# Kernel optimization log

Hardware: AMD Instinct MI355X
Metric: run time of the kernel (lower is better)

The kernel has to match this reference:

```python
import jax, jax.numpy as jnp
import numpy as np

IN_F = 8192
OUT_F = 8192
TOKENS = 4096
QP = 127.0   # 2**(8-1) - 1
QN = -128.0  # -2**(8-1)


def setup_inputs() -> dict:
    key = jax.random.key(0)
    k1, k2 = jax.random.split(key)
    x = jax.random.normal(k1, (TOKENS, IN_F), dtype=jnp.float32)
    # torch.randint(0, 2, ...) -> values in {0, 1}
    weight = jax.random.randint(k2, (OUT_F, IN_F), 0, 2, dtype=jnp.int32)
    weight_scale = jnp.ones((1,), dtype=jnp.float32)
    bias = jnp.zeros((OUT_F,), dtype=jnp.float32)
    return {"x": x, "weight": weight, "weight_scale": weight_scale, "bias": bias}


def reference(x, weight, weight_scale, bias):
    # activation_quant: per-row symmetric int8 quantization
    s = QP / jnp.clip(jnp.max(jnp.abs(x), axis=-1, keepdims=True), 1e-5)  # [T,1]
    x_q = jnp.clip(jnp.round(x * s), QN, QP)  # int8 values held in f32 (exact)
    y = jnp.einsum('tk,nk->tn', x_q, weight.astype(x.dtype))  # [T, OUT_F]
    # post_quant_process: dequantize by activation scale then weight scale
    out = y / s / weight_scale
    return out + bias[None, :]
```

## Files before the change

### kernel.cpp

```cpp
#include <hip/hip_runtime.h>

#define TOKENS 4096
#define IN_F   8192
#define OUT_F  8192

typedef int v4i __attribute__((ext_vector_type(4)));

__device__ __forceinline__ void gload_lds16(const void* g, void* l) {
    __builtin_amdgcn_global_load_lds(
        (const __attribute__((address_space(1))) void*)g,
        (__attribute__((address_space(3))) void*)l, 16, 0, 0);
}

__global__ __launch_bounds__(256) void quant_kernel(const float* __restrict__ x,
                                                    signed char* __restrict__ xq,
                                                    float* __restrict__ recip_s) {
    const int row = blockIdx.x;
    const int t   = threadIdx.x;
    const float4* xr = (const float4*)(x + (size_t)row * IN_F);
    float4 v[8];
    float m = 0.f;
#pragma unroll
    for (int i = 0; i < 8; ++i) {
        v[i] = xr[t + 256 * i];
        m = fmaxf(m, fmaxf(fmaxf(fabsf(v[i].x), fabsf(v[i].y)),
                           fmaxf(fabsf(v[i].z), fabsf(v[i].w))));
    }
#pragma unroll
    for (int off = 32; off > 0; off >>= 1)
        m = fmaxf(m, __shfl_xor(m, off));
    __shared__ float wmax[4];
    if ((t & 63) == 0) wmax[t >> 6] = m;
    __syncthreads();
    m = fmaxf(fmaxf(wmax[0], wmax[1]), fmaxf(wmax[2], wmax[3]));
    m = fmaxf(m, 1e-5f);
    const float s = 127.0f / m;
    if (t == 0) recip_s[row] = m / 127.0f;
    unsigned int* out = (unsigned int*)(xq + (size_t)row * IN_F);
#pragma unroll
    for (int i = 0; i < 8; ++i) {
        int a = (int)fminf(fmaxf(rintf(v[i].x * s), -128.f), 127.f);
        int b = (int)fminf(fmaxf(rintf(v[i].y * s), -128.f), 127.f);
        int c = (int)fminf(fmaxf(rintf(v[i].z * s), -128.f), 127.f);
        int d = (int)fminf(fmaxf(rintf(v[i].w * s), -128.f), 127.f);
        out[t + 256 * i] = (a & 255) | ((b & 255) << 8) | ((c & 255) << 16) | ((d & 255) << 24);
    }
}

__global__ __launch_bounds__(256) void pack_w(const int* __restrict__ w,
                                              unsigned int* __restrict__ w8) {
    const size_t idx = (size_t)blockIdx.x * 256 + threadIdx.x;
    int4 a = ((const int4*)w)[idx];
    w8[idx] = (a.x & 255) | ((a.y & 255) << 8) | ((a.z & 255) << 16) | ((a.w & 255) << 24);
}

__global__ __launch_bounds__(256, 2) void gemm_kernel(const signed char* __restrict__ A,
                                                      const signed char* __restrict__ B,
                                                      const float* __restrict__ recip_s,
                                                      const float* __restrict__ wscale,
                                                      const float* __restrict__ bias,
                                                      float* __restrict__ out) {
    __shared__ signed char As[128 * 64];
    __shared__ signed char Bs[256 * 64];
    const int t    = threadIdx.x;
    const int wave = t >> 6;
    const int lane = t & 63;
    const int m0 = blockIdx.y * 128;
    const int n0 = blockIdx.x * 256;
    const int wm = (wave >> 1) * 64;
    const int wn = (wave & 1) * 128;

    v4i acc[4][8] = {};

    const int rowS = t >> 2;
    const int colS = ((t & 3) ^ ((t >> 3) & 3)) * 16;
    const signed char* gA = A + (size_t)(m0 + rowS) * IN_F + colS;
    const signed char* gB = B + (size_t)(n0 + rowS) * IN_F + colS;
    signed char* lA = As + t * 16;
    signed char* lB = Bs + t * 16;

    const int r16 = lane & 15;
    const int q   = lane >> 4;
    const int cOff = ((q ^ ((r16 >> 1) & 3)) * 16);

    for (int k0 = 0; k0 < IN_F; k0 += 64) {
        gload_lds16(gA + k0, lA);
        gload_lds16(gA + (size_t)64 * IN_F + k0, lA + 4096);
        gload_lds16(gB + k0, lB);
        gload_lds16(gB + (size_t)64 * IN_F + k0, lB + 4096);
        gload_lds16(gB + (size_t)128 * IN_F + k0, lB + 8192);
        gload_lds16(gB + (size_t)192 * IN_F + k0, lB + 12288);
        __syncthreads();

        v4i a[4], b[8];
#pragma unroll
        for (int i = 0; i < 4; ++i)
            a[i] = *(const v4i*)(As + (wm + i * 16 + r16) * 64 + cOff);
#pragma unroll
        for (int j = 0; j < 8; ++j)
            b[j] = *(const v4i*)(Bs + (wn + j * 16 + r16) * 64 + cOff);
#pragma unroll
        for (int i = 0; i < 4; ++i)
#pragma unroll
            for (int j = 0; j < 8; ++j)
                acc[i][j] = __builtin_amdgcn_mfma_i32_16x16x64_i8(a[i], b[j], acc[i][j], 0, 0, 0);
        __syncthreads();
    }

    const float rws = 1.0f / wscale[0];
#pragma unroll
    for (int i = 0; i < 4; ++i) {
#pragma unroll
        for (int r = 0; r < 4; ++r) {
            const int row = m0 + wm + i * 16 + q * 4 + r;
            const float rs = recip_s[row] * rws;
#pragma unroll
            for (int j = 0; j < 8; ++j) {
                const int col = n0 + wn + j * 16 + r16;
                out[(size_t)row * OUT_F + col] = (float)acc[i][j][r] * rs + bias[col];
            }
        }
    }
}

extern "C" void kernel_launch(void* const* d_in, const int* in_sizes, int n_in,
                              void* d_out, int out_size, void* d_ws, size_t ws_size,
                              hipStream_t stream) {
    const float* x      = (const float*)d_in[0];
    const int*   w      = (const int*)d_in[1];
    const float* wscale = (const float*)d_in[2];
    const float* bias   = (const float*)d_in[3];
    float* out = (float*)d_out;

    signed char* xq = (signed char*)d_ws;
    signed char* w8 = xq + (size_t)TOKENS * IN_F;
    float* recip_s  = (float*)(w8 + (size_t)OUT_F * IN_F);

    quant_kernel<<<TOKENS, 256, 0, stream>>>(x, xq, recip_s);
    pack_w<<<(int)(((size_t)OUT_F * IN_F) / 4 / 256), 256, 0, stream>>>(w, (unsigned int*)w8);
    dim3 grid(OUT_F / 256, TOKENS / 128);
    gemm_kernel<<<grid, 256, 0, stream>>>(xq, w8, recip_s, wscale, bias, out);
}
```

Before: 736.8 us.

## Triple-buffer LDS tiles to overlap global loads with MFMA compute

Replaces the single-buffered load, barrier, compute, barrier loop with a three-stage LDS ring. Global-to-LDS loads for tile k+2 are issued while tile k is being computed, and partial vmcnt waits plus one barrier per stage replace the two full barriers per iteration. It also raises wave priority around the MFMA block. LDS use per block grows to 72 KB, which with two blocks per CU is still within LDS capacity. The hand-written vmcnt accounting is fragile if the load count per stage changes.

```diff
diff --git a/kernel.cpp b/kernel.cpp
--- a/kernel.cpp
+++ b/kernel.cpp
@@ -3,6 +3,9 @@
 #define TOKENS 4096
 #define IN_F   8192
 #define OUT_F  8192
+#define BK     64
+#define TILEB  24576
+#define NT     (IN_F / BK)
 
 typedef int v4i __attribute__((ext_vector_type(4)));
 
@@ -60,8 +63,7 @@
                                                       const float* __restrict__ wscale,
                                                       const float* __restrict__ bias,
                                                       float* __restrict__ out) {
-    __shared__ signed char As[128 * 64];
-    __shared__ signed char Bs[256 * 64];
+    __shared__ signed char smem[3 * TILEB];
     const int t    = threadIdx.x;
     const int wave = t >> 6;
     const int lane = t & 63;
@@ -76,36 +78,67 @@
     const int colS = ((t & 3) ^ ((t >> 3) & 3)) * 16;
     const signed char* gA = A + (size_t)(m0 + rowS) * IN_F + colS;
     const signed char* gB = B + (size_t)(n0 + rowS) * IN_F + colS;
-    signed char* lA = As + t * 16;
-    signed char* lB = Bs + t * 16;
 
     const int r16 = lane & 15;
     const int q   = lane >> 4;
     const int cOff = ((q ^ ((r16 >> 1) & 3)) * 16);
 
-    for (int k0 = 0; k0 < IN_F; k0 += 64) {
-        gload_lds16(gA + k0, lA);
-        gload_lds16(gA + (size_t)64 * IN_F + k0, lA + 4096);
-        gload_lds16(gB + k0, lB);
-        gload_lds16(gB + (size_t)64 * IN_F + k0, lB + 4096);
-        gload_lds16(gB + (size_t)128 * IN_F + k0, lB + 8192);
-        gload_lds16(gB + (size_t)192 * IN_F + k0, lB + 12288);
-        __syncthreads();
+#define STAGE(kt, buf) do {                                                  \
+        signed char* lA = smem + (buf) * TILEB + t * 16;                     \
+        signed char* lB = lA + 8192;                                         \
+        const size_t k0 = (size_t)(kt) * BK;                                 \
+        gload_lds16(gA + k0, lA);                                            \
+        gload_lds16(gA + (size_t)64  * IN_F + k0, lA + 4096);                \
+        gload_lds16(gB + k0, lB);                                            \
+        gload_lds16(gB + (size_t)64  * IN_F + k0, lB + 4096);                \
+        gload_lds16(gB + (size_t)128 * IN_F + k0, lB + 8192);                \
+        gload_lds16(gB + (size_t)192 * IN_F + k0, lB + 12288);               \
+    } while (0)
 
-        v4i a[4], b[8];
-#pragma unroll
-        for (int i = 0; i < 4; ++i)
-            a[i] = *(const v4i*)(As + (wm + i * 16 + r16) * 64 + cOff);
-#pragma unroll
-        for (int j = 0; j < 8; ++j)
-            b[j] = *(const v4i*)(Bs + (wn + j * 16 + r16) * 64 + cOff);
-#pragma unroll
-        for (int i = 0; i < 4; ++i)
-#pragma unroll
-            for (int j = 0; j < 8; ++j)
-                acc[i][j] = __builtin_amdgcn_mfma_i32_16x16x64_i8(a[i], b[j], acc[i][j], 0, 0, 0);
-        __syncthreads();
+#define COMPUTE(buf) do {                                                    \
+        const signed char* As_ = smem + (buf) * TILEB;                       \
+        const signed char* Bs_ = As_ + 8192;                                 \
+        v4i a[4], b[8];                                                      \
+        _Pragma("unroll")                                                    \
+        for (int i = 0; i < 4; ++i)                                          \
+            a[i] = *(const v4i*)(As_ + (wm + i * 16 + r16) * 64 + cOff);     \
+        _Pragma("unroll")                                                    \
+        for (int j = 0; j < 8; ++j)                                          \
+            b[j] = *(const v4i*)(Bs_ + (wn + j * 16 + r16) * 64 + cOff);     \
+        __builtin_amdgcn_s_setprio(1);                                       \
+        _Pragma("unroll")                                                    \
+        for (int i = 0; i < 4; ++i)                                          \
+            _Pragma("unroll")                                                \
+            for (int j = 0; j < 8; ++j)                                      \
+                acc[i][j] = __builtin_amdgcn_mfma_i32_16x16x64_i8(           \
+                    a[i], b[j], acc[i][j], 0, 0, 0);                         \
+        __builtin_amdgcn_s_setprio(0);                                       \
+    } while (0)
+
+#define WAITBAR(N) do {                                                      \
+        asm volatile("s_waitcnt vmcnt(" #N ")" ::: "memory");                \
+        __builtin_amdgcn_s_barrier();                                        \
+        asm volatile("" ::: "memory");                                       \
+    } while (0)
+
+    STAGE(0, 0);
+    asm volatile("s_waitcnt vmcnt(0)" ::: "memory");
+    STAGE(1, 1);
+    __builtin_amdgcn_s_barrier();
+    asm volatile("" ::: "memory");
+
+    for (int kt = 0; kt < NT - 2; kt += 3) {
+        STAGE(kt + 2, 2); COMPUTE(0); WAITBAR(6);
+        STAGE(kt + 3, 0); COMPUTE(1); WAITBAR(6);
+        STAGE(kt + 4, 1); COMPUTE(2); WAITBAR(6);
     }
+    COMPUTE(0);
+    WAITBAR(0);
+    COMPUTE(1);
+
+#undef STAGE
+#undef COMPUTE
+#undef WAITBAR
 
     const float rws = 1.0f / wscale[0];
 #pragma unroll
```

Result: faster. 699.1 us (-5.1%).
